# Kernel optimization log

Hardware: AMD Instinct MI355X
Metric: run time of the kernel (lower is better)

## Reference

```python
import jax, jax.numpy as jnp
import numpy as np

GRID_RES = 128
SCALE = 2.0
DEFORM_SCALE = 1.0
N_VERTS = 200_000
N_TETS = 1_000_000

TRI_TABLE = np.array([
    [-1,-1,-1,-1,-1,-1],[1,0,2,-1,-1,-1],[4,0,3,-1,-1,-1],[1,4,2,1,3,4],
    [3,1,5,-1,-1,-1],[2,3,0,2,5,3],[1,4,0,1,5,4],[4,2,5,-1,-1,-1],
    [4,5,2,-1,-1,-1],[4,1,0,4,5,1],[3,2,0,3,5,2],[1,3,5,-1,-1,-1],
    [4,1,2,4,3,1],[3,0,4,-1,-1,-1],[2,0,1,-1,-1,-1],[-1,-1,-1,-1,-1,-1]], dtype=np.int64)
NUM_TRI_TABLE = np.array([0,1,1,2,1,2,2,1,1,2,2,1,2,1,1,0], dtype=np.int64)
BASE_TET_EDGES = np.array([0,1,0,2,0,3,1,2,1,3,2,3], dtype=np.int64)


def setup_inputs() -> dict:
    key = jax.random.key(0)
    k1, k2, k3, k4 = jax.random.split(key, 4)
    verts = jax.random.normal(k1, (N_VERTS, 3), dtype=jnp.float32) * SCALE
    deform = jax.random.normal(k2, (N_VERTS, 3), dtype=jnp.float32)
    sdf_sign = jnp.sign(jax.random.normal(k3, (N_VERTS,), dtype=jnp.float32) + 1e-8)
    sdf_sign = jnp.where(sdf_sign == 0, 1.0, sdf_sign)
    sdf_abs = jnp.ones((N_VERTS,), dtype=jnp.float32)
    indices = jax.random.randint(k4, (N_TETS, 4), 0, N_VERTS, dtype=jnp.int64)
    return dict(verts=verts, deform=deform, sdf_sign=sdf_sign, sdf_abs=sdf_abs, indices=indices)


def _prep_topology(sdf_np, tet_np):
    """Non-differentiable (torch.no_grad) integer bookkeeping, done in numpy."""
    occ = sdf_np > 0                       # [N]
    occ_fx4 = occ[tet_np]                  # [T,4]
    occ_sum = occ_fx4.sum(-1)
    valid = (occ_sum > 0) & (occ_sum < 4)
    tet_v = tet_np[valid]                  # [Tv,4]
    all_edges = tet_v[:, BASE_TET_EDGES].reshape(-1, 2)
    all_edges = np.sort(all_edges, axis=1)     # same as torch sort_edges (min,max)
    unique_edges, idx_map = np.unique(all_edges, axis=0, return_inverse=True)
    idx_map = idx_map.reshape(-1)
    mask_edges = occ[unique_edges].sum(-1) == 1   # sign-crossing edges
    mapping = np.full(unique_edges.shape[0], -1, dtype=np.int64)
    mapping[mask_edges] = np.arange(int(mask_edges.sum()), dtype=np.int64)
    idx_map = mapping[idx_map].reshape(-1, 6)
    interp_v = unique_edges[mask_edges]            # [M,2]
    tetindex = (occ_fx4[valid].astype(np.int64) * np.array([1, 2, 4, 8])).sum(-1)
    num_tri = NUM_TRI_TABLE[tetindex]
    one, two = num_tri == 1, num_tri == 2
    f1 = np.take_along_axis(idx_map[one], TRI_TABLE[tetindex[one]][:, :3], axis=1).reshape(-1, 3)
    f2 = np.take_along_axis(idx_map[two], TRI_TABLE[tetindex[two]][:, :6], axis=1).reshape(-1, 3)
    faces = np.concatenate([f1, f2], axis=0)
    tet_gidx = np.arange(tet_np.shape[0], dtype=np.int64)[valid]
    fg1 = tet_gidx[one] * 2
    g2 = tet_gidx[two]
    fg2 = np.stack([g2 * 2, g2 * 2 + 1], axis=-1).reshape(-1)
    face_gidx = np.concatenate([fg1, fg2], axis=0)
    return interp_v, faces, face_gidx


def _map_uv(face_gidx, max_idx):
    Ng = int(np.ceil(np.sqrt((max_idx + 1) // 2)))
    lin = np.linspace(0.0, 1.0 - 1.0 / Ng, Ng, dtype=np.float32)
    tex_y, tex_x = np.meshgrid(lin, lin, indexing='ij')
    pad = np.float32(0.9 / Ng)
    uvs = np.stack([tex_x, tex_y, tex_x + pad, tex_y,
                    tex_x + pad, tex_y + pad, tex_x, tex_y + pad], axis=-1).reshape(-1, 2)
    raw = face_gidx // 2
    tet_idx = (raw // Ng) * Ng + (raw % Ng)
    tri_idx = face_gidx % 2
    uv_idx = np.stack([tet_idx * 4, tet_idx * 4 + tri_idx + 1, tet_idx * 4 + tri_idx + 2], axis=-1).reshape(-1, 3)
    return jnp.asarray(uvs), jnp.asarray(uv_idx)


def reference(verts, deform, sdf_sign, sdf_abs, indices):
    sdf = sdf_sign * jnp.abs(sdf_abs)                      # [N]
    v_deformed = verts + (2.0 / (GRID_RES * 2)) * deform * DEFORM_SCALE
    interp_v, faces, face_gidx = _prep_topology(np.asarray(sdf), np.asarray(indices))
    iv = jnp.asarray(interp_v)                             # [M,2]
    pos = v_deformed[iv]                                   # [M,2,3]
    s = sdf[iv]                                            # [M,2]
    sa, sb = s[:, 0], s[:, 1]
    denom = sa - sb                                        # == sa + (-sb)
    # torch: weights = flip([sa,-sb]) / denom -> [-sb, sa] / (sa - sb)
    out_verts = pos[:, 0] * (-sb / denom)[:, None] + pos[:, 1] * (sa / denom)[:, None]
    uvs, uv_idx = _map_uv(face_gidx, indices.shape[0] * 2)
    return out_verts, jnp.asarray(faces), uvs, uv_idx
```

## Files before the change

### kernel.cpp

```cpp
#include <hip/hip_runtime.h>
#include <stdint.h>

#define NVERT 200000
#define NTET  1000000
#define NE2   3200000
#define NG 1000
#define PAYB 23
#define PAYMASK ((1u<<PAYB)-1u)
#define KB 18
#define KMASK ((1u<<KB)-1u)

#define SCAN_T 256
#define SCAN_E 16
#define SCAN_EPB (SCAN_T*SCAN_E)

__constant__ int c_tri[16][6] = {
  {-1,-1,-1,-1,-1,-1},{1,0,2,-1,-1,-1},{4,0,3,-1,-1,-1},{1,4,2,1,3,4},
  {3,1,5,-1,-1,-1},{2,3,0,2,5,3},{1,4,0,1,5,4},{4,2,5,-1,-1,-1},
  {4,5,2,-1,-1,-1},{4,1,0,4,5,1},{3,2,0,3,5,2},{1,3,5,-1,-1,-1},
  {4,1,2,4,3,1},{3,0,4,-1,-1,-1},{2,0,1,-1,-1,-1},{-1,-1,-1,-1,-1,-1}};
__constant__ int c_ntri[16] = {0,1,1,2,1,2,2,1,1,2,2,1,2,1,1,0};
__constant__ int c_e0[6] = {0,0,0,1,1,2};
__constant__ int c_e1[6] = {1,2,3,2,3,3};

__device__ __forceinline__ uint64_t shfl64(uint64_t x, int src){
  int lo = __shfl((int)(uint32_t)x, src, 64);
  int hi = __shfl((int)(uint32_t)(x >> 32), src, 64);
  return ((uint64_t)(uint32_t)hi << 32) | (uint32_t)lo;
}

__global__ void k_init(const float* __restrict__ ssign, const float* __restrict__ sabs,
                       float* __restrict__ sdf, uint8_t* __restrict__ occ,
                       uint32_t* __restrict__ bincl, uint32_t* __restrict__ fill){
  int i = blockIdx.x*blockDim.x + threadIdx.x;
  if (i >= NVERT) return;
  float s = ssign[i] * fabsf(sabs[i]);
  sdf[i] = s;
  occ[i] = (s > 0.0f) ? 1 : 0;
  bincl[i] = 0u;
  fill[i]  = 0u;
}

__global__ void k_tet(const int* __restrict__ idx, const uint8_t* __restrict__ occ,
                      uint8_t* __restrict__ tetidx, uint64_t* __restrict__ oneTwo,
                      uint32_t* __restrict__ bcnt){
  int t = blockIdx.x*blockDim.x + threadIdx.x;
  if (t >= NTET) return;
  int v[4];
  #pragma unroll
  for (int j = 0; j < 4; ++j) v[j] = idx[t*4+j];
  int ti = 0;
  #pragma unroll
  for (int j = 0; j < 4; ++j) ti |= (occ[v[j]] ? 1 : 0) << j;
  tetidx[t] = (uint8_t)ti;
  int nt = c_ntri[ti];
  oneTwo[t] = ((nt == 1) ? 1ull : 0ull) | (((nt == 2) ? 1ull : 0ull) << 32);
  if (nt == 0) return;
  #pragma unroll
  for (int e = 0; e < 6; ++e){
    int o0 = (ti >> c_e0[e]) & 1, o1 = (ti >> c_e1[e]) & 1;
    if (o0 == o1) continue;
    int a = v[c_e0[e]], b = v[c_e1[e]];
    if (a > b){ int tmp = a; a = b; b = tmp; }
    atomicAdd((unsigned int*)&bcnt[a], 1u);
  }
}

__global__ void k_scan_block(uint32_t* __restrict__ d, uint32_t* __restrict__ part, int L){
  int tid = threadIdx.x;
  int base = blockIdx.x*SCAN_EPB + tid*SCAN_E;
  uint32_t v[SCAN_E];
  #pragma unroll
  for (int j = 0; j < SCAN_E; ++j){
    int i = base + j;
    v[j] = (i < L) ? d[i] : 0u;
  }
  #pragma unroll
  for (int j = 1; j < SCAN_E; ++j) v[j] += v[j-1];
  __shared__ uint32_t s[SCAN_T];
  s[tid] = v[SCAN_E-1];
  __syncthreads();
  for (int o = 1; o < SCAN_T; o <<= 1){
    uint32_t x = (tid >= o) ? s[tid-o] : 0u;
    __syncthreads();
    s[tid] += x;
    __syncthreads();
  }
  uint32_t off = s[tid] - v[SCAN_E-1];
  #pragma unroll
  for (int j = 0; j < SCAN_E; ++j){
    int i = base + j;
    if (i < L) d[i] = v[j] + off;
  }
  if (tid == SCAN_T-1 && part) part[blockIdx.x] = s[SCAN_T-1];
}

__global__ void k_scan_part(uint32_t* __restrict__ part, int n){
  int tid = threadIdx.x;
  int per = (n + SCAN_T - 1)/SCAN_T;
  int st = tid*per, en = st + per; if (en > n) en = n;
  uint32_t sum = 0;
  for (int i = st; i < en; ++i) sum += part[i];
  __shared__ uint32_t s[SCAN_T];
  s[tid] = sum;
  __syncthreads();
  for (int o = 1; o < SCAN_T; o <<= 1){
    uint32_t x = (tid >= o) ? s[tid-o] : 0u;
    __syncthreads();
    s[tid] += x;
    __syncthreads();
  }
  uint32_t off = s[tid] - sum;
  uint32_t run = off;
  for (int i = st; i < en; ++i){ run += part[i]; part[i] = run; }
}

__global__ void k_scan_add(uint32_t* __restrict__ d, const uint32_t* __restrict__ part, int L){
  int blk = blockIdx.x;
  if (blk == 0) return;
  uint32_t off = part[blk-1];
  int base = blk*SCAN_EPB;
  #pragma unroll
  for (int j = 0; j < SCAN_E; ++j){
    int i = base + j*SCAN_T + threadIdx.x;
    if (i < L) d[i] += off;
  }
}

__global__ void k_scan_block64(uint64_t* __restrict__ d, uint64_t* __restrict__ part, int L){
  int tid = threadIdx.x;
  int base = blockIdx.x*SCAN_EPB + tid*SCAN_E;
  uint64_t v[SCAN_E];
  #pragma unroll
  for (int j = 0; j < SCAN_E; ++j){
    int i = base + j;
    v[j] = (i < L) ? d[i] : 0ull;
  }
  #pragma unroll
  for (int j = 1; j < SCAN_E; ++j) v[j] += v[j-1];
  __shared__ uint64_t s[SCAN_T];
  s[tid] = v[SCAN_E-1];
  __syncthreads();
  for (int o = 1; o < SCAN_T; o <<= 1){
    uint64_t x = (tid >= o) ? s[tid-o] : 0ull;
    __syncthreads();
    s[tid] += x;
    __syncthreads();
  }
  uint64_t off = s[tid] - v[SCAN_E-1];
  #pragma unroll
  for (int j = 0; j < SCAN_E; ++j){
    int i = base + j;
    if (i < L) d[i] = v[j] + off;
  }
  if (tid == SCAN_T-1 && part) part[blockIdx.x] = s[SCAN_T-1];
}

__global__ void k_scan_part64(uint64_t* __restrict__ part, int n){
  int tid = threadIdx.x;
  int per = (n + SCAN_T - 1)/SCAN_T;
  int st = tid*per, en = st + per; if (en > n) en = n;
  uint64_t sum = 0;
  for (int i = st; i < en; ++i) sum += part[i];
  __shared__ uint64_t s[SCAN_T];
  s[tid] = sum;
  __syncthreads();
  for (int o = 1; o < SCAN_T; o <<= 1){
    uint64_t x = (tid >= o) ? s[tid-o] : 0ull;
    __syncthreads();
    s[tid] += x;
    __syncthreads();
  }
  uint64_t off = s[tid] - sum;
  uint64_t run = off;
  for (int i = st; i < en; ++i){ run += part[i]; part[i] = run; }
}

__global__ void k_scan_add64(uint64_t* __restrict__ d, const uint64_t* __restrict__ part, int L){
  int blk = blockIdx.x;
  if (blk == 0) return;
  uint64_t off = part[blk-1];
  int base = blk*SCAN_EPB;
  #pragma unroll
  for (int j = 0; j < SCAN_E; ++j){
    int i = base + j*SCAN_T + threadIdx.x;
    if (i < L) d[i] += off;
  }
}

__global__ void k_scatter(const int* __restrict__ idx, const uint8_t* __restrict__ tetidx,
                          const uint32_t* __restrict__ bincl, uint32_t* __restrict__ fill,
                          uint64_t* __restrict__ skey){
  int t = blockIdx.x*blockDim.x + threadIdx.x;
  if (t >= NTET) return;
  int ti = tetidx[t];
  if (c_ntri[ti] == 0) return;
  int v[4];
  #pragma unroll
  for (int j = 0; j < 4; ++j) v[j] = idx[t*4+j];
  #pragma unroll
  for (int e = 0; e < 6; ++e){
    int o0 = (ti >> c_e0[e]) & 1, o1 = (ti >> c_e1[e]) & 1;
    if (o0 == o1) continue;
    int a = v[c_e0[e]], b = v[c_e1[e]];
    if (a > b){ int tmp = a; a = b; b = tmp; }
    uint32_t base = (a > 0) ? bincl[a-1] : 0u;
    uint32_t p = base + atomicAdd((unsigned int*)&fill[a], 1u);
    if (p < NE2)
      skey[p] = ((uint64_t)(uint32_t)a << (PAYB+KB)) | ((uint64_t)(uint32_t)b << PAYB)
              | (uint32_t)(t*6 + e);
  }
}

__global__ void k_bsort(uint64_t* __restrict__ skey, const uint32_t* __restrict__ bincl,
                        uint32_t* __restrict__ maskA){
  int gid  = blockIdx.x*blockDim.x + threadIdx.x;
  int w    = gid >> 6;
  int lane = threadIdx.x & 63;
  int W    = (gridDim.x*blockDim.x) >> 6;
  for (int b = w; b < NVERT; b += W){
    uint32_t s0 = (b > 0) ? bincl[b-1] : 0u;
    uint32_t e0 = bincl[b];
    int n = (int)(e0 - s0);
    if (n <= 0) continue;
    if (n == 1){
      if (lane == 0) maskA[s0] = 1u;
      continue;
    }
    if (n <= 64){
      uint64_t ki = (lane < n) ? skey[s0+lane] : ~0ull;
      int r = 0; bool dup = false;
      for (int j = 0; j < n; ++j){
        uint64_t kj = shfl64(ki, j);
        bool lt = (kj < ki);
        r += lt ? 1 : 0;
        dup |= lt && ((kj >> PAYB) == (ki >> PAYB));
      }
      if (lane < n){
        skey[s0 + r] = ki;
        maskA[s0 + r] = dup ? 0u : 1u;
      }
    } else if (n <= 128){
      int n2 = n - 64;
      uint64_t k0 = skey[s0+lane];
      uint64_t k1 = (lane < n2) ? skey[s0+64+lane] : ~0ull;
      int r0 = 0, r1 = 0; bool d0 = false, d1 = false;
      for (int j = 0; j < 64; ++j){
        uint64_t kj = shfl64(k0, j);
        bool lt0 = (kj < k0);
        r0 += lt0 ? 1 : 0;  d0 |= lt0 && ((kj >> PAYB) == (k0 >> PAYB));
        bool lt1 = (kj < k1);
        r1 += lt1 ? 1 : 0;  d1 |= lt1 && ((kj >> PAYB) == (k1 >> PAYB));
      }
      for (int j = 0; j < n2; ++j){
        uint64_t kj = shfl64(k1, j);
        bool lt0 = (kj < k0);
        r0 += lt0 ? 1 : 0;  d0 |= lt0 && ((kj >> PAYB) == (k0 >> PAYB));
        bool lt1 = (kj < k1);
        r1 += lt1 ? 1 : 0;  d1 |= lt1 && ((kj >> PAYB) == (k1 >> PAYB));
      }
      { skey[s0 + r0] = k0; maskA[s0 + r0] = d0 ? 0u : 1u; }
      if (lane < n2){ skey[s0 + r1] = k1; maskA[s0 + r1] = d1 ? 0u : 1u; }
    } else if (lane == 0){
      for (int i = 1; i < n; ++i){
        uint64_t x = skey[s0+i];
        int j = i-1;
        while (j >= 0 && skey[s0+j] > x){ skey[s0+j+1] = skey[s0+j]; --j; }
        skey[s0+j+1] = x;
      }
      maskA[s0] = 1u;
      for (int i = 1; i < n; ++i)
        maskA[s0+i] = ((skey[s0+i] >> PAYB) != (skey[s0+i-1] >> PAYB)) ? 1u : 0u;
    }
  }
}

__global__ void k_emit(const uint64_t* __restrict__ skey, const uint32_t* __restrict__ maskI,
                       const uint32_t* __restrict__ bincl,
                       const float* __restrict__ verts, const float* __restrict__ deform,
                       const float* __restrict__ sdf,
                       uint32_t* __restrict__ edge2vert, float* __restrict__ out){
  int i = blockIdx.x*blockDim.x + threadIdx.x;
  if (i >= NE2) return;
  uint32_t nE = (uint32_t)__builtin_amdgcn_readfirstlane((int)bincl[NVERT-1]);
  if ((uint32_t)i >= nE) return;
  uint64_t k = skey[i];
  uint32_t m = maskI[i];
  uint32_t pm = (i > 0) ? maskI[i-1] : 0u;
  uint32_t vid = m - 1u;
  edge2vert[(uint32_t)(k & PAYMASK)] = vid;
  if (m == pm) return;
  int a = (int)(k >> (PAYB+KB)), b = (int)((k >> PAYB) & KMASK);
  float sa = sdf[a], sb = sdf[b];
  float denom = sa - sb;
  float w0 = __fdiv_rn(-sb, denom);
  float w1 = __fdiv_rn(sa, denom);
  #pragma unroll
  for (int c = 0; c < 3; ++c){
    float pa = __fadd_rn(verts[a*3+c], __fmul_rn(0.0078125f, deform[a*3+c]));
    float pb = __fadd_rn(verts[b*3+c], __fmul_rn(0.0078125f, deform[b*3+c]));
    out[(size_t)vid*3 + c] = __fadd_rn(__fmul_rn(pa, w0), __fmul_rn(pb, w1));
  }
}

__global__ void k_faces(const uint8_t* __restrict__ tetidx,
                        const uint64_t* __restrict__ oneTwoI,
                        const uint32_t* __restrict__ maskI, const uint32_t* __restrict__ bincl,
                        const uint32_t* __restrict__ edge2vert, float* __restrict__ out){
  int t = blockIdx.x*blockDim.x + threadIdx.x;
  if (t >= NTET) return;
  int ti = tetidx[t];
  int nt = c_ntri[ti];
  if (nt == 0) return;
  uint32_t nE      = (uint32_t)__builtin_amdgcn_readfirstlane((int)bincl[NVERT-1]);
  uint32_t nInterp = (uint32_t)__builtin_amdgcn_readfirstlane((int)maskI[nE-1]);
  uint64_t totOT   = oneTwoI[NTET-1];
  uint32_t nOne    = (uint32_t)__builtin_amdgcn_readfirstlane((int)(uint32_t)totOT);
  uint32_t nTwo    = (uint32_t)__builtin_amdgcn_readfirstlane((int)(uint32_t)(totOT >> 32));
  size_t facesOff = (size_t)3*nInterp;
  size_t nFaces = (size_t)nOne + 2u*(size_t)nTwo;
  size_t uvIdxOff = facesOff + 3*nFaces + (size_t)(4*NG*NG)*2;
  uint64_t ot = oneTwoI[t];
  uint32_t oneR = (uint32_t)ot, twoR = (uint32_t)(ot >> 32);
  for (int k = 0; k < nt; ++k){
    size_t row = (nt == 1) ? (size_t)(oneR-1u)
                           : (size_t)nOne + 2u*(size_t)(twoR-1u) + (size_t)k;
    #pragma unroll
    for (int j = 0; j < 3; ++j){
      int e = c_tri[ti][k*3+j];
      out[facesOff + row*3 + j] = (float)edge2vert[t*6 + e];
    }
    int tri = (nt == 2) ? k : 0;
    long long t4 = 4LL*t;
    out[uvIdxOff + row*3 + 0] = (float)t4;
    out[uvIdxOff + row*3 + 1] = (float)(t4 + tri + 1);
    out[uvIdxOff + row*3 + 2] = (float)(t4 + tri + 2);
  }
}

__global__ void k_uvs(const uint32_t* __restrict__ maskI, const uint32_t* __restrict__ bincl,
                      const uint64_t* __restrict__ oneTwoI, float* __restrict__ out){
  int r = blockIdx.x*blockDim.x + threadIdx.x;
  if (r >= 4*NG*NG) return;
  uint32_t nE      = (uint32_t)__builtin_amdgcn_readfirstlane((int)bincl[NVERT-1]);
  uint32_t nInterp = (uint32_t)__builtin_amdgcn_readfirstlane((int)maskI[nE-1]);
  uint64_t totOT   = oneTwoI[NTET-1];
  uint32_t nOne    = (uint32_t)__builtin_amdgcn_readfirstlane((int)(uint32_t)totOT);
  uint32_t nTwo    = (uint32_t)__builtin_amdgcn_readfirstlane((int)(uint32_t)(totOT >> 32));
  size_t uvOff = (size_t)3*nInterp + 3*((size_t)nOne + 2u*(size_t)nTwo);
  int cell = r >> 2, c = r & 3;
  int iy = cell / NG, jx = cell % NG;
  const double step = (1.0 - 1.0/NG)/(NG-1);
  float x = (jx == NG-1) ? (float)(1.0 - 1.0/NG) : (float)((double)jx*step);
  float y = (iy == NG-1) ? (float)(1.0 - 1.0/NG) : (float)((double)iy*step);
  float pad = (float)(0.9/NG);
  float u, vv;
  switch (c){
    case 0: u = x;                 vv = y;                 break;
    case 1: u = __fadd_rn(x, pad); vv = y;                 break;
    case 2: u = __fadd_rn(x, pad); vv = __fadd_rn(y, pad); break;
    default:u = x;                 vv = __fadd_rn(y, pad); break;
  }
  out[uvOff + (size_t)r*2 + 0] = u;
  out[uvOff + (size_t)r*2 + 1] = vv;
}

static void scan_u32(uint32_t* d, int L, uint32_t* part, hipStream_t s){
  int nb = (L + SCAN_EPB - 1)/SCAN_EPB;
  k_scan_block<<<nb, SCAN_T, 0, s>>>(d, part, L);
  if (nb > 1){
    k_scan_part<<<1, SCAN_T, 0, s>>>(part, nb);
    k_scan_add<<<nb, SCAN_T, 0, s>>>(d, part, L);
  }
}

static void scan_u64(uint64_t* d, int L, uint64_t* part, hipStream_t s){
  int nb = (L + SCAN_EPB - 1)/SCAN_EPB;
  k_scan_block64<<<nb, SCAN_T, 0, s>>>(d, part, L);
  if (nb > 1){
    k_scan_part64<<<1, SCAN_T, 0, s>>>(part, nb);
    k_scan_add64<<<nb, SCAN_T, 0, s>>>(d, part, L);
  }
}

extern "C" void kernel_launch(void* const* d_in, const int* in_sizes, int n_in,
                              void* d_out, int out_size, void* d_ws, size_t ws_size,
                              hipStream_t stream){
  const float* verts  = (const float*)d_in[0];
  const float* deform = (const float*)d_in[1];
  const float* ssign  = (const float*)d_in[2];
  const float* sabs   = (const float*)d_in[3];
  const int*   idx    = (const int*)d_in[4];
  float* out = (float*)d_out;

  char* ws = (char*)d_ws;
  size_t o = 0;
  auto alloc = [&](size_t bytes) -> void* {
    void* p = ws + o;
    o = (o + bytes + 255) & ~(size_t)255;
    return p;
  };
  float*    sdf     = (float*)   alloc(sizeof(float)*NVERT);
  uint8_t*  occ     = (uint8_t*) alloc(NVERT);
  uint8_t*  tetidx  = (uint8_t*) alloc(NTET);
  uint32_t* bincl   = (uint32_t*)alloc(sizeof(uint32_t)*NVERT);
  uint32_t* fill    = (uint32_t*)alloc(sizeof(uint32_t)*NVERT);
  uint64_t* oneTwo  = (uint64_t*)alloc(sizeof(uint64_t)*NTET);
  uint32_t* maskI   = (uint32_t*)alloc(sizeof(uint32_t)*NE2);
  uint64_t* skey    = (uint64_t*)alloc(sizeof(uint64_t)*NE2);
  uint32_t* e2v     = (uint32_t*)alloc(sizeof(uint32_t)*NTET*6);
  uint32_t* part    = (uint32_t*)alloc(sizeof(uint32_t)*2048);
  uint64_t* part64  = (uint64_t*)alloc(sizeof(uint64_t)*2048);
  if (o > ws_size) return;

  k_init<<<(NVERT+255)/256, 256, 0, stream>>>(ssign, sabs, sdf, occ, bincl, fill);
  k_tet<<<(NTET+255)/256, 256, 0, stream>>>(idx, occ, tetidx, oneTwo, bincl);

  scan_u32(bincl, NVERT, part, stream);

  k_scatter<<<(NTET+255)/256, 256, 0, stream>>>(idx, tetidx, bincl, fill, skey);
  k_bsort<<<1024, 256, 0, stream>>>(skey, bincl, maskI);

  scan_u32(maskI, NE2, part, stream);
  scan_u64(oneTwo, NTET, part64, stream);

  k_emit<<<(NE2+255)/256, 256, 0, stream>>>(skey, maskI, bincl, verts, deform, sdf, e2v, out);
  k_faces<<<(NTET+255)/256, 256, 0, stream>>>(tetidx, oneTwo, maskI, bincl, e2v, out);
  k_uvs<<<(4*NG*NG+255)/256, 256, 0, stream>>>(maskI, bincl, oneTwo, out);
}
```

Baseline: 652.1 us.

## Replace random edge scatter with two-pass coarse-bin then per-vertex placement

The direct scatter of edge keys to per-vertex buckets via global atomics is split into two passes. First, each block histograms its keys into coarse bins (8192 vertices each) in shared memory and writes them as contiguous chunks to a staging buffer. Second, one block per bin places the keys into their final per-vertex slots, so the scattered writes land in a localized region. The staging buffer is aliased with the maskI/e2v storage to save workspace, and tet index loads become int4 vector loads; the cost is an extra pass over roughly 3.2M keys plus block-level synchronization.

```diff
diff --git a/kernel.cpp b/kernel.cpp
--- a/kernel.cpp
+++ b/kernel.cpp
@@ -9,6 +9,8 @@
 #define PAYMASK ((1u<<PAYB)-1u)
 #define KB 18
 #define KMASK ((1u<<KB)-1u)
+#define BSH 13
+#define NBIN ((NVERT + (1<<BSH) - 1) >> BSH)
 
 #define SCAN_T 256
 #define SCAN_E 16
@@ -31,7 +33,8 @@
 
 __global__ void k_init(const float* __restrict__ ssign, const float* __restrict__ sabs,
                        float* __restrict__ sdf, uint8_t* __restrict__ occ,
-                       uint32_t* __restrict__ bincl, uint32_t* __restrict__ fill){
+                       uint32_t* __restrict__ bincl, uint32_t* __restrict__ fill,
+                       uint32_t* __restrict__ binFill){
   int i = blockIdx.x*blockDim.x + threadIdx.x;
   if (i >= NVERT) return;
   float s = ssign[i] * fabsf(sabs[i]);
@@ -39,6 +42,7 @@
   occ[i] = (s > 0.0f) ? 1 : 0;
   bincl[i] = 0u;
   fill[i]  = 0u;
+  if (i < NBIN) binFill[i] = 0u;
 }
 
 __global__ void k_tet(const int* __restrict__ idx, const uint8_t* __restrict__ occ,
@@ -46,9 +50,8 @@
                       uint32_t* __restrict__ bcnt){
   int t = blockIdx.x*blockDim.x + threadIdx.x;
   if (t >= NTET) return;
-  int v[4];
-  #pragma unroll
-  for (int j = 0; j < 4; ++j) v[j] = idx[t*4+j];
+  int4 vv = *(const int4*)&idx[t*4];
+  int v[4] = {vv.x, vv.y, vv.z, vv.w};
   int ti = 0;
   #pragma unroll
   for (int j = 0; j < 4; ++j) ti |= (occ[v[j]] ? 1 : 0) << j;
@@ -188,27 +191,79 @@
   }
 }
 
-__global__ void k_scatter(const int* __restrict__ idx, const uint8_t* __restrict__ tetidx,
-                          const uint32_t* __restrict__ bincl, uint32_t* __restrict__ fill,
-                          uint64_t* __restrict__ skey){
-  int t = blockIdx.x*blockDim.x + threadIdx.x;
-  if (t >= NTET) return;
-  int ti = tetidx[t];
-  if (c_ntri[ti] == 0) return;
-  int v[4];
-  #pragma unroll
-  for (int j = 0; j < 4; ++j) v[j] = idx[t*4+j];
+__global__ void __launch_bounds__(256) k_binscat(const int* __restrict__ idx,
+                          const uint8_t* __restrict__ tetidx,
+                          const uint32_t* __restrict__ bincl, uint32_t* __restrict__ binFill,
+                          uint64_t* __restrict__ skeyBin){
+  __shared__ uint32_t hist[NBIN];
+  __shared__ uint32_t offs[NBIN];
+  __shared__ uint32_t gdest[NBIN];
+  __shared__ uint64_t stK[1536];
+  __shared__ uint32_t stD[1536];
+  int tid = threadIdx.x;
+  int t = blockIdx.x*256 + tid;
+  if (tid < NBIN) hist[tid] = 0u;
+  __syncthreads();
+  bool val[6]; uint64_t key[6]; int bin[6]; uint32_t rnk[6];
+  int ti = (t < NTET) ? tetidx[t] : 0;
+  #pragma unroll
+  for (int e = 0; e < 6; ++e){ val[e] = false; key[e] = 0; bin[e] = 0; rnk[e] = 0; }
+  if (c_ntri[ti] != 0){
+    int4 vv = *(const int4*)&idx[t*4];
+    int v[4] = {vv.x, vv.y, vv.z, vv.w};
+    #pragma unroll
+    for (int e = 0; e < 6; ++e){
+      int o0 = (ti >> c_e0[e]) & 1, o1 = (ti >> c_e1[e]) & 1;
+      if (o0 == o1) continue;
+      int a = v[c_e0[e]], b = v[c_e1[e]];
+      if (a > b){ int tmp = a; a = b; b = tmp; }
+      val[e] = true;
+      key[e] = ((uint64_t)(uint32_t)a << (PAYB+KB)) | ((uint64_t)(uint32_t)b << PAYB)
+             | (uint32_t)(t*6 + e);
+      bin[e] = a >> BSH;
+    }
+  }
+  #pragma unroll
+  for (int e = 0; e < 6; ++e)
+    if (val[e]) rnk[e] = atomicAdd(&hist[bin[e]], 1u);
+  __syncthreads();
+  if (tid == 0){
+    uint32_t run = 0;
+    for (int b2 = 0; b2 < NBIN; ++b2){ offs[b2] = run; run += hist[b2]; }
+  }
+  __syncthreads();
+  if (tid < NBIN && hist[tid] > 0){
+    uint32_t seg = (tid > 0) ? bincl[((uint32_t)tid << BSH) - 1] : 0u;
+    gdest[tid] = seg + atomicAdd(&binFill[tid], hist[tid]);
+  }
+  __syncthreads();
   #pragma unroll
   for (int e = 0; e < 6; ++e){
-    int o0 = (ti >> c_e0[e]) & 1, o1 = (ti >> c_e1[e]) & 1;
-    if (o0 == o1) continue;
-    int a = v[c_e0[e]], b = v[c_e1[e]];
-    if (a > b){ int tmp = a; a = b; b = tmp; }
+    if (!val[e]) continue;
+    uint32_t o = offs[bin[e]] + rnk[e];
+    stK[o] = key[e];
+    stD[o] = gdest[bin[e]] + rnk[e];
+  }
+  __syncthreads();
+  uint32_t total = offs[NBIN-1] + hist[NBIN-1];
+  for (uint32_t i = tid; i < total; i += 256){
+    uint32_t d = stD[i];
+    if (d < NE2) skeyBin[d] = stK[i];
+  }
+}
+
+__global__ void k_place(const uint64_t* __restrict__ skeyBin, const uint32_t* __restrict__ bincl,
+                        uint32_t* __restrict__ fill, uint64_t* __restrict__ skey){
+  int b = blockIdx.x;
+  uint32_t s = (b > 0) ? bincl[((uint32_t)b << BSH) - 1] : 0u;
+  uint32_t hiA = (((uint32_t)b + 1u) << BSH) - 1u; if (hiA > NVERT-1) hiA = NVERT-1;
+  uint32_t e = bincl[hiA];
+  for (uint32_t i = s + threadIdx.x; i < e; i += blockDim.x){
+    uint64_t k = skeyBin[i];
+    uint32_t a = (uint32_t)(k >> (PAYB+KB));
     uint32_t base = (a > 0) ? bincl[a-1] : 0u;
-    uint32_t p = base + atomicAdd((unsigned int*)&fill[a], 1u);
-    if (p < NE2)
-      skey[p] = ((uint64_t)(uint32_t)a << (PAYB+KB)) | ((uint64_t)(uint32_t)b << PAYB)
-              | (uint32_t)(t*6 + e);
+    uint32_t p = base + atomicAdd(&fill[a], 1u);
+    if (p < NE2) skey[p] = k;
   }
 }
 
@@ -405,20 +460,25 @@
   uint8_t*  tetidx  = (uint8_t*) alloc(NTET);
   uint32_t* bincl   = (uint32_t*)alloc(sizeof(uint32_t)*NVERT);
   uint32_t* fill    = (uint32_t*)alloc(sizeof(uint32_t)*NVERT);
+  uint32_t* binFill = (uint32_t*)alloc(sizeof(uint32_t)*64);
   uint64_t* oneTwo  = (uint64_t*)alloc(sizeof(uint64_t)*NTET);
-  uint32_t* maskI   = (uint32_t*)alloc(sizeof(uint32_t)*NE2);
+  size_t unionBytes = sizeof(uint32_t)*NE2 + sizeof(uint32_t)*NTET*6;
+  char* unionBase   = (char*)alloc(unionBytes);
+  uint64_t* skeyBin = (uint64_t*)unionBase;
+  uint32_t* maskI   = (uint32_t*)unionBase;
+  uint32_t* e2v     = (uint32_t*)(unionBase + sizeof(uint32_t)*NE2);
   uint64_t* skey    = (uint64_t*)alloc(sizeof(uint64_t)*NE2);
-  uint32_t* e2v     = (uint32_t*)alloc(sizeof(uint32_t)*NTET*6);
   uint32_t* part    = (uint32_t*)alloc(sizeof(uint32_t)*2048);
   uint64_t* part64  = (uint64_t*)alloc(sizeof(uint64_t)*2048);
   if (o > ws_size) return;
 
-  k_init<<<(NVERT+255)/256, 256, 0, stream>>>(ssign, sabs, sdf, occ, bincl, fill);
+  k_init<<<(NVERT+255)/256, 256, 0, stream>>>(ssign, sabs, sdf, occ, bincl, fill, binFill);
   k_tet<<<(NTET+255)/256, 256, 0, stream>>>(idx, occ, tetidx, oneTwo, bincl);
 
   scan_u32(bincl, NVERT, part, stream);
 
-  k_scatter<<<(NTET+255)/256, 256, 0, stream>>>(idx, tetidx, bincl, fill, skey);
+  k_binscat<<<(NTET+255)/256, 256, 0, stream>>>(idx, tetidx, bincl, binFill, skeyBin);
+  k_place<<<NBIN, 1024, 0, stream>>>(skeyBin, bincl, fill, skey);
   k_bsort<<<1024, 256, 0, stream>>>(skey, bincl, maskI);
 
   scan_u32(maskI, NE2, part, stream);
```

Result: slower. 1.376 ms (+111.0%).
